# Kernel tuning notes

Hardware: AMD Instinct MI355X
Metric: run time of the kernel (lower is better)

## Reference

```python
import jax, jax.numpy as jnp
import numpy as np
import math

NX = 1024
N_HEAD = 16
HEAD_DIM = NX // N_HEAD
N_CTX = 2048
REL_VOCAB = 64
B = 2
S = 2048


def setup_inputs() -> dict:
    key = jax.random.key(0)
    ks = jax.random.split(key, 7)
    x = jax.random.normal(ks[0], (B, S, NX), dtype=jnp.float32)
    rel = jax.random.randint(ks[1], (B, S, S), 0, REL_VOCAB, dtype=jnp.int64)
    sc = 0.02
    Wqkv = jax.random.normal(ks[2], (NX, 3 * NX), dtype=jnp.float32) * sc
    bqkv = jnp.zeros((3 * NX,), dtype=jnp.float32)
    Wproj = jax.random.normal(ks[3], (NX, NX), dtype=jnp.float32) * sc
    bproj = jnp.zeros((NX,), dtype=jnp.float32)
    rel_emb = jax.random.normal(ks[4], (REL_VOCAB, N_HEAD), dtype=jnp.float32) * sc
    return {"x": x, "Wqkv": Wqkv, "bqkv": bqkv, "Wproj": Wproj,
            "bproj": bproj, "rel_emb": rel_emb, "rel": rel}


def reference(x, Wqkv, bqkv, Wproj, bproj, rel_emb, rel):
    Bsz, Sq, _ = x.shape
    qkv = x @ Wqkv + bqkv                      # [B,S,3*nx]
    q, k, v = jnp.split(qkv, 3, axis=-1)
    def split_heads(t):                        # [B,S,nx] -> [B,H,S,D]
        return t.reshape(Bsz, Sq, N_HEAD, HEAD_DIM).transpose(0, 2, 1, 3)
    q, k, v = split_heads(q), split_heads(k), split_heads(v)
    w = jnp.einsum('bhqd,bhkd->bhqk', q, k) / math.sqrt(HEAD_DIM)
    bmask = jnp.tril(jnp.ones((Sq, Sq), dtype=w.dtype))[None, None]  # [1,1,S,S]
    w = w * bmask - 1e10 * (1.0 - bmask)
    relw = rel_emb[rel].transpose(0, 3, 1, 2)  # [B,S,S,H] -> [B,H,S,S]
    w = w * (relw * bmask)                     # faithful: masked scores become 0
    p = jax.nn.softmax(w, axis=-1)
    a = jnp.einsum('bhqk,bhkd->bhqd', p, v)
    a = a.transpose(0, 2, 1, 3).reshape(Bsz, Sq, NX)  # merge heads
    return a @ Wproj + bproj
```

## Files before the change

### kernel.cpp

```cpp
#include <hip/hip_runtime.h>

typedef unsigned short u16;
typedef unsigned char u8;
typedef __attribute__((ext_vector_type(8))) short short8;
typedef __attribute__((ext_vector_type(4))) short short4v;
typedef __attribute__((ext_vector_type(4))) float f32x4;

#define GLD16(g, l) __builtin_amdgcn_global_load_lds( \
    (const __attribute__((address_space(1))) void*)(g), \
    (__attribute__((address_space(3))) void*)(l), 16, 0, 0)

__device__ __forceinline__ float bf2f(u16 u){
  union { unsigned int i; float f; } v; v.i = ((unsigned int)u) << 16; return v.f;
}
__device__ __forceinline__ u16 f2bf(float f){
  union { float f; unsigned int i; } v; v.f = f;
  unsigned int u = v.i;
  unsigned int r = (u + 0x7FFFu + ((u >> 16) & 1u)) >> 16;
  return (u16)r;
}

__device__ __forceinline__ f32x4 mfma16(short4v a, short4v b, f32x4 c){
#if __has_builtin(__builtin_amdgcn_mfma_f32_16x16x16bf16_1k)
  return __builtin_amdgcn_mfma_f32_16x16x16bf16_1k(a, b, c, 0, 0, 0);
#else
  asm volatile("s_nop 1\n\tv_mfma_f32_16x16x16_bf16 %0, %1, %2, %0" : "+v"(c) : "v"(a), "v"(b));
  return c;
#endif
}

__global__ __launch_bounds__(256) void prep_k(const float* __restrict__ x, u16* __restrict__ xb,
                                              const float* __restrict__ Wqkv, u16* __restrict__ wqkvT,
                                              const float* __restrict__ Wproj, u16* __restrict__ wprojT,
                                              const int* __restrict__ rel, u8* __restrict__ rel8){
  const int bid = blockIdx.x, t = threadIdx.x;
  if (bid < 4096){
    int i = bid * 256 + t;
    float4 v = ((const float4*)x)[i];
    unsigned long long pk = (unsigned long long)f2bf(v.x)
      | ((unsigned long long)f2bf(v.y) << 16)
      | ((unsigned long long)f2bf(v.z) << 32)
      | ((unsigned long long)f2bf(v.w) << 48);
    ((unsigned long long*)xb)[i] = pk;
  } else if (bid < 8192){
    const float* W; u16* Wt; int K, N, blk, nbx;
    if (bid < 7168){ W = Wqkv; Wt = wqkvT; K = 1024; N = 3072; blk = bid - 4096; nbx = 96; }
    else           { W = Wproj; Wt = wprojT; K = 1024; N = 1024; blk = bid - 7168; nbx = 32; }
    __shared__ float tl[32][33];
    int n0 = (blk % nbx) * 32, k0 = (blk / nbx) * 32;
    int tx = t & 31, ty = t >> 5;
    for (int i = ty; i < 32; i += 8)
      tl[i][tx] = W[(size_t)(k0 + i) * N + n0 + tx];
    __syncthreads();
    for (int i = ty; i < 32; i += 8)
      Wt[(size_t)(n0 + i) * K + k0 + tx] = f2bf(tl[tx][i]);
  } else {
    int i = (bid - 8192) * 256 + t;
    int4 v = ((const int4*)rel)[i];
    unsigned int pk = (unsigned int)(v.x & 255) | ((unsigned int)(v.y & 255) << 8)
      | ((unsigned int)(v.z & 255) << 16) | ((unsigned int)(v.w & 255) << 24);
    ((unsigned int*)rel8)[i] = pk;
  }
}

__global__ __launch_bounds__(256) void gemm_qkv_k(const u16* __restrict__ A, const u16* __restrict__ Bt,
                                                  const float* __restrict__ bias,
                                                  u16* __restrict__ oq, u16* __restrict__ okk, u16* __restrict__ vt){
  __shared__ u16 la[3][128 * 32];
  __shared__ u16 lb[3][128 * 32];
  const int K = 1024;
  const int t = threadIdx.x, w = t >> 6, lane = t & 63;
  const int l15 = lane & 15, l4 = lane >> 4;
  const int m0 = blockIdx.y * 128, n0 = blockIdx.x * 128;
  const int wr = w >> 1, wc = w & 1;
  f32x4 acc[4][4] = {};
  const u16* Abase = A + (size_t)m0 * K;
  const u16* Bbase = Bt + (size_t)n0 * K;

  const int srow0 = t >> 2, srow1 = 64 + (t >> 2);
  const int cg = t & 3;
  const int sc0 = cg ^ (srow0 & 3), sc1 = cg ^ (srow1 & 3);
  const int wbase0 = (w * 64) * 8, wbase1 = (256 + w * 64) * 8;

#define QSTAGE(kt, buf) do {                                                        \
    GLD16(Abase + (size_t)srow0 * K + (kt) * 32 + sc0 * 8, &la[buf][wbase0]);       \
    GLD16(Abase + (size_t)srow1 * K + (kt) * 32 + sc1 * 8, &la[buf][wbase1]);       \
    GLD16(Bbase + (size_t)srow0 * K + (kt) * 32 + sc0 * 8, &lb[buf][wbase0]);       \
    GLD16(Bbase + (size_t)srow1 * K + (kt) * 32 + sc1 * 8, &lb[buf][wbase1]);       \
  } while (0)

  QSTAGE(0, 0);
  QSTAGE(1, 1);
  for (int ki = 0; ki < 32; ++ki){
    __builtin_amdgcn_sched_barrier(0);
    if (ki < 31) asm volatile("s_waitcnt vmcnt(4)" ::: "memory");
    else         asm volatile("s_waitcnt vmcnt(0)" ::: "memory");
    __builtin_amdgcn_s_barrier();
    __builtin_amdgcn_sched_barrier(0);
    if (ki + 2 < 32) QSTAGE(ki + 2, (ki + 2) % 3);
    const int cb = ki % 3;
    short8 af[4], bfr[4];
#pragma unroll
    for (int mi = 0; mi < 4; ++mi){
      int row = wr * 64 + mi * 16 + l15;
      af[mi] = *(const short8*)&la[cb][row * 32 + ((l4 ^ (row & 3)) * 8)];
    }
#pragma unroll
    for (int ni = 0; ni < 4; ++ni){
      int row = wc * 64 + ni * 16 + l15;
      bfr[ni] = *(const short8*)&lb[cb][row * 32 + ((l4 ^ (row & 3)) * 8)];
    }
    __builtin_amdgcn_s_setprio(1);
#pragma unroll
    for (int mi = 0; mi < 4; ++mi)
#pragma unroll
      for (int ni = 0; ni < 4; ++ni)
        acc[mi][ni] = __builtin_amdgcn_mfma_f32_16x16x32_bf16(af[mi], bfr[ni], acc[mi][ni], 0, 0, 0);
    __builtin_amdgcn_s_setprio(0);
  }
#undef QSTAGE

#pragma unroll
  for (int mi = 0; mi < 4; ++mi){
    const int m_base = m0 + wr * 64 + mi * 16 + l4 * 4;
    const int bsel = m_base >> 11, s0q = m_base & 2047;
#pragma unroll
    for (int ni = 0; ni < 4; ++ni){
      int n = n0 + wc * 64 + ni * 16 + l15;
      float vb = bias[n];
      int tt = n >> 10, rr = n & 1023, head = rr >> 6, dd = rr & 63;
      if (tt == 2){
        int c = s0q >> 6, w6 = s0q & 63;
        int pj0 = (((w6 >> 2) & 3) << 4) | (((w6 >> 4) & 3) << 2);
        u16 o4[4];
#pragma unroll
        for (int r = 0; r < 4; ++r) o4[r] = f2bf(acc[mi][ni][r] + vb);
        *(uint2*)(vt + ((size_t)(bsel * 16 + head) * 64 + dd) * 2048 + c * 64 + pj0) = *(const uint2*)o4;
      } else {
        u16* dst = (tt == 0) ? oq : okk;
#pragma unroll
        for (int r = 0; r < 4; ++r)
          dst[(((size_t)(bsel * 16 + head)) * 2048 + s0q + r) * 64 + dd] = f2bf(acc[mi][ni][r] + vb);
      }
    }
  }
}

template<int BN>
__global__ __launch_bounds__(256) void gemm_bt_k(const u16* __restrict__ A, const u16* __restrict__ Bt,
                                                 const float* __restrict__ bias, float* __restrict__ of,
                                                 int M, int N, int K){
  __shared__ u16 la[128 * 64];
  __shared__ u16 lb[BN * 64];
  const int t = threadIdx.x, w = t >> 6, lane = t & 63;
  const int l15 = lane & 15, l4 = lane >> 4;
  const int m0 = blockIdx.y * 128, n0 = blockIdx.x * BN;
  const int wr = w >> 1, wc = w & 1;
  constexpr int NI = BN / 32;
  f32x4 acc[4][NI] = {};
  const u16* Abase = A + (size_t)m0 * K;
  const u16* Bbase = Bt + (size_t)n0 * K;
  for (int kt = 0; kt < K; kt += 64){
    __syncthreads();
#pragma unroll
    for (int i = 0; i < 4; ++i){
      int chunk = i * 256 + t;
      int row = chunk >> 3, cs = chunk & 7;
      int c = cs ^ (row & 7);
      GLD16(Abase + (size_t)row * K + kt + c * 8, &la[(i * 256 + w * 64) * 8]);
    }
#pragma unroll
    for (int i = 0; i < BN / 32; ++i){
      int chunk = i * 256 + t;
      int row = chunk >> 3, cs = chunk & 7;
      int c = cs ^ (row & 7);
      GLD16(Bbase + (size_t)row * K + kt + c * 8, &lb[(i * 256 + w * 64) * 8]);
    }
    asm volatile("s_waitcnt vmcnt(0)" ::: "memory");
    __syncthreads();
    short8 af[4][2], bfr[NI][2];
#pragma unroll
    for (int mi = 0; mi < 4; ++mi){
      int row = wr * 64 + mi * 16 + l15;
#pragma unroll
      for (int h = 0; h < 2; ++h)
        af[mi][h] = *(const short8*)&la[row * 64 + (((h * 4 + l4) ^ (row & 7)) * 8)];
    }
#pragma unroll
    for (int ni = 0; ni < NI; ++ni){
      int row = wc * (BN / 2) + ni * 16 + l15;
#pragma unroll
      for (int h = 0; h < 2; ++h)
        bfr[ni][h] = *(const short8*)&lb[row * 64 + (((h * 4 + l4) ^ (row & 7)) * 8)];
    }
#pragma unroll
    for (int mi = 0; mi < 4; ++mi)
#pragma unroll
      for (int ni = 0; ni < NI; ++ni){
        acc[mi][ni] = __builtin_amdgcn_mfma_f32_16x16x32_bf16(af[mi][0], bfr[ni][0], acc[mi][ni], 0, 0, 0);
        acc[mi][ni] = __builtin_amdgcn_mfma_f32_16x16x32_bf16(af[mi][1], bfr[ni][1], acc[mi][ni], 0, 0, 0);
      }
  }
#pragma unroll
  for (int mi = 0; mi < 4; ++mi){
#pragma unroll
    for (int ni = 0; ni < NI; ++ni){
#pragma unroll
      for (int r = 0; r < 4; ++r){
        int m = m0 + wr * 64 + mi * 16 + l4 * 4 + r;
        int n = n0 + wc * (BN / 2) + ni * 16 + l15;
        of[(size_t)m * N + n] = acc[mi][ni][r] + bias[n];
      }
    }
  }
}

__global__ __launch_bounds__(256) void vsuf2_k(const u16* __restrict__ vt, float* __restrict__ vsuf){
  __shared__ float part[32][64];
  const int bh = blockIdx.x;
  const int d = threadIdx.x & 63, qtr = threadIdx.x >> 6;
  const u16* row = vt + ((size_t)bh * 64 + d) * 2048;
  for (int c = qtr * 8; c < qtr * 8 + 8; ++c){
    float s = 0.f;
#pragma unroll
    for (int jv = 0; jv < 8; ++jv){
      short8 v = *(const short8*)(row + c * 64 + jv * 8);
#pragma unroll
      for (int e = 0; e < 8; ++e) s += bf2f((u16)v[e]);
    }
    part[c][d] = s;
  }
  __syncthreads();
  if (threadIdx.x < 64){
    float run = 0.f;
    vsuf[((size_t)bh * 33 + 32) * 64 + d] = 0.f;
    for (int c = 31; c >= 0; --c){
      run += part[c][d];
      vsuf[((size_t)bh * 33 + c) * 64 + d] = run;
    }
  }
}

template<int U8, int SPLIT>
__global__ __launch_bounds__(256, 4) void attn_k(const u16* __restrict__ qb, const u16* __restrict__ kb,
                                                 const u16* __restrict__ vt, const float* __restrict__ vsuf,
                                                 const void* __restrict__ relp, const float* __restrict__ rel_emb,
                                                 u16* __restrict__ ab, float* __restrict__ pacc,
                                                 float* __restrict__ prsum){
  __shared__ u16 Kt[2][64 * 64];
  __shared__ u16 Vt[2][64 * 64];
  __shared__ float remb[64];
  int p, hf, bh;
  if (SPLIT){
    const int lid = blockIdx.x;
    const int bhgrp = lid & 7, within = (lid >> 3) & 3, pf = lid >> 5;
    bh = bhgrp * 4 + within;
    p = pf >> 1; hf = pf & 1;
  } else {
    p = blockIdx.x; hf = 0; bh = blockIdx.y;
  }
  const int b = bh >> 4, h = bh & 15;
  const int TA = p, TB = 31 - p;
  const int q0A = TA * 64, q0B = TB * 64;
  const int tid = threadIdx.x, w = tid >> 6, lane = tid & 63;
  const int l15 = lane & 15, l4 = lane >> 4;
  if (tid < 64) remb[tid] = rel_emb[tid * 16 + h] * (0.125f * 1.44269504088896f);
  const u16* kbh = kb + ((size_t)bh * 2048) * 64;
  const u16* vbh = vt + ((size_t)bh * 64) * 2048;
  const u16* qA = qb + (((size_t)bh * 2048) + q0A + w * 16 + l15) * 64 + l4 * 8;
  const u16* qB = qb + (((size_t)bh * 2048) + q0B + w * 16 + l15) * 64 + l4 * 8;
  const short8 aqA0 = *(const short8*)qA, aqA1 = *(const short8*)(qA + 32);
  const short8 aqB0 = *(const short8*)qB, aqB1 = *(const short8*)(qB + 32);
  const u8*  r8A  = (const u8*)relp + ((size_t)b * 2048 + q0A + w * 16 + l15) * 2048;
  const u8*  r8B  = (const u8*)relp + ((size_t)b * 2048 + q0B + w * 16 + l15) * 2048;
  const int* r32A = (const int*)relp + ((size_t)b * 2048 + q0A + w * 16 + l15) * 2048;
  const int* r32B = (const int*)relp + ((size_t)b * 2048 + q0B + w * 16 + l15) * 2048;

  const int srow0 = (tid >> 3), srow1 = 32 + (tid >> 3);
  const int scs = tid & 7;
  const int sc0 = scs ^ (srow0 & 7), sc1 = scs ^ (srow1 & 7);
  const int sldsoff = (w * 64) * 8;

#define STAGE(ktile, buf) do {                                                       \
    GLD16(kbh + (size_t)((ktile) * 64 + srow0) * 64 + sc0 * 8, &Kt[buf][sldsoff]);   \
    GLD16(kbh + (size_t)((ktile) * 64 + srow1) * 64 + sc1 * 8, &Kt[buf][2048 + sldsoff]); \
    GLD16(vbh + (size_t)srow0 * 2048 + (ktile) * 64 + sc0 * 8, &Vt[buf][sldsoff]);   \
    GLD16(vbh + (size_t)srow1 * 2048 + (ktile) * 64 + sc1 * 8, &Vt[buf][2048 + sldsoff]); \
  } while (0)

  f32x4 acc[4] = {};
  float rsum = 0.f;
  unsigned int relc[4], reln[4];

  auto relload = [&](bool isA, int kt, unsigned int* dst){
    int off = kt * 64 + 4 * l4;
    if (U8){
      const u8* pp = isA ? r8A : r8B;
#pragma unroll
      for (int t = 0; t < 4; ++t) dst[t] = *(const unsigned int*)(pp + off + 16 * t);
    } else {
      const int* pp = isA ? r32A : r32B;
#pragma unroll
      for (int t = 0; t < 4; ++t){
        int4 v4 = *(const int4*)(pp + off + 16 * t);
        dst[t] = (unsigned int)(v4.x & 255) | ((unsigned int)(v4.y & 255) << 8)
               | ((unsigned int)(v4.z & 255) << 16) | ((unsigned int)(v4.w & 255) << 24);
      }
    }
  };

  auto writeout = [&](int Td, int q0){
    asm volatile("s_nop 7\n\ts_nop 7" :::);
    float s = rsum;
    s += __shfl_xor(s, 16);
    s += __shfl_xor(s, 32);
    float invZ = 1.f / (s + (float)(2048 - (Td + 1) * 64));
    int qg = q0 + w * 16 + l15;
    const float* sufp = vsuf + ((size_t)bh * 33 + Td + 1) * 64;
#pragma unroll
    for (int ni = 0; ni < 4; ++ni){
      float4 sv = *(const float4*)(sufp + ni * 16 + 4 * l4);
      unsigned int lo2 = (unsigned int)f2bf((acc[ni][0] + sv.x) * invZ)
                       | ((unsigned int)f2bf((acc[ni][1] + sv.y) * invZ) << 16);
      unsigned int hi2 = (unsigned int)f2bf((acc[ni][2] + sv.z) * invZ)
                       | ((unsigned int)f2bf((acc[ni][3] + sv.w) * invZ) << 16);
      uint2 o; o.x = lo2; o.y = hi2;
      *(uint2*)(ab + ((size_t)b * 2048 + qg) * 1024 + h * 64 + ni * 16 + 4 * l4) = o;
    }
  };

  const int lo = (SPLIT && hf) ? 17 : 0;
  const int hi = (SPLIT && !hf) ? 17 : 33;

  {
    bool isA0 = (lo <= TA);
    int kt0 = isA0 ? lo : lo - TA - 1;
    STAGE(kt0, 0);
    relload(isA0, kt0, relc);
  }

  for (int it = lo; it < hi; ++it){
    const bool isA = (it <= TA);
    const int kt = isA ? it : (it - TA - 1);
    const int cur = (it - lo) & 1;

    __builtin_amdgcn_sched_barrier(0);
    asm volatile("s_waitcnt vmcnt(4)" ::: "memory");
    __builtin_amdgcn_s_barrier();
    __builtin_amdgcn_sched_barrier(0);

    if (it + 1 < hi){
      const bool nA = (it + 1 <= TA);
      const int nkt = nA ? (it + 1) : (it - TA);
      STAGE(nkt, cur ^ 1);
      relload(nA, nkt, reln);
    }

    const short8 a0 = isA ? aqA0 : aqB0;
    const short8 a1 = isA ? aqA1 : aqB1;
    const bool diag = (kt == (isA ? TA : TB));

    short4v pk[4];
    __builtin_amdgcn_s_setprio(1);
#pragma unroll
    for (int t = 0; t < 4; ++t){
      const int krow = 16 * t + l15;
      const u16* kbase = &Kt[cur][krow * 64];
      short8 bk0 = *(const short8*)&kbase[((l4)     ^ (krow & 7)) * 8];
      short8 bk1 = *(const short8*)&kbase[((4 + l4) ^ (krow & 7)) * 8];
      f32x4 sf = {0.f, 0.f, 0.f, 0.f};
      sf = __builtin_amdgcn_mfma_f32_16x16x32_bf16(bk0, a0, sf, 0, 0, 0);
      sf = __builtin_amdgcn_mfma_f32_16x16x32_bf16(bk1, a1, sf, 0, 0, 0);
      unsigned int rw = relc[t];
      const int kk = 16 * t + 4 * l4;
      float prv[4];
#pragma unroll
      for (int r = 0; r < 4; ++r){
        float sc = sf[r] * remb[(rw >> (8 * r)) & 255];
        if (diag) sc = (kk + r <= w * 16 + l15) ? sc : 0.f;
        float pv = __builtin_amdgcn_exp2f(sc);
        rsum += pv;
        prv[r] = pv;
      }
      union { unsigned int u[2]; short4v s; } pu;
      asm("v_cvt_pk_bf16_f32 %0, %1, %2" : "=v"(pu.u[0]) : "v"(prv[0]), "v"(prv[1]));
      asm("v_cvt_pk_bf16_f32 %0, %1, %2" : "=v"(pu.u[1]) : "v"(prv[2]), "v"(prv[3]));
      pk[t] = pu.s;
    }
    asm volatile("s_nop 2" :::);
#pragma unroll
    for (int ni = 0; ni < 4; ++ni){
      const int drow = ni * 16 + l15;
      const u16* vbase = &Vt[cur][drow * 64];
      short8 vv0 = *(const short8*)&vbase[(((2 * l4)     ^ (drow & 7))) * 8];
      short8 vv1 = *(const short8*)&vbase[(((2 * l4 + 1) ^ (drow & 7))) * 8];
      short4v va0 = {vv0[0], vv0[1], vv0[2], vv0[3]};
      short4v va1 = {vv0[4], vv0[5], vv0[6], vv0[7]};
      short4v va2 = {vv1[0], vv1[1], vv1[2], vv1[3]};
      short4v va3 = {vv1[4], vv1[5], vv1[6], vv1[7]};
      acc[ni] = mfma16(va0, pk[0], acc[ni]);
      acc[ni] = mfma16(va1, pk[1], acc[ni]);
      acc[ni] = mfma16(va2, pk[2], acc[ni]);
      acc[ni] = mfma16(va3, pk[3], acc[ni]);
    }
    __builtin_amdgcn_s_setprio(0);

    if (it == TA){
      writeout(TA, q0A);
#pragma unroll
      for (int ni = 0; ni < 4; ++ni) acc[ni] = f32x4{0.f, 0.f, 0.f, 0.f};
      rsum = 0.f;
    }
    if (it + 1 < hi){
#pragma unroll
      for (int t = 0; t < 4; ++t) relc[t] = reln[t];
    }
  }
#undef STAGE

  if (SPLIT){
    asm volatile("s_nop 7\n\ts_nop 7" :::);
    float s = rsum;
    s += __shfl_xor(s, 16);
    s += __shfl_xor(s, 32);
    const size_t slot = (((size_t)bh * 16 + p) * 2 + hf);
    float* pslot = pacc + slot * 4096;
#pragma unroll
    for (int ni = 0; ni < 4; ++ni)
      *(f32x4*)(pslot + (w * 16 + l15) * 64 + ni * 16 + 4 * l4) = acc[ni];
    if (l4 == 0) prsum[slot * 64 + w * 16 + l15] = s;
  } else {
    writeout(TB, q0B);
  }
}

__global__ __launch_bounds__(256) void attn_fin_k(const float* __restrict__ pacc,
                                                  const float* __restrict__ prsum,
                                                  const float* __restrict__ vsuf,
                                                  u16* __restrict__ ab){
  const int p = blockIdx.x, bh = blockIdx.y;
  const int b = bh >> 4, h = bh & 15;
  const int TB = 31 - p, q0 = TB * 64;
  const int r = threadIdx.x >> 2, cg = threadIdx.x & 3;
  const size_t slot = ((size_t)bh * 16 + p) * 2;
  const size_t base = slot * 4096 + r * 64 + cg * 16;
  float rs = prsum[slot * 64 + r] + prsum[(slot + 1) * 64 + r];
  float invZ = 1.f / (rs + (float)(2048 - (TB + 1) * 64));
  const float* sufp = vsuf + ((size_t)bh * 33 + TB + 1) * 64 + cg * 16;
  u16 o[16];
#pragma unroll
  for (int j = 0; j < 4; ++j){
    f32x4 a0 = *(const f32x4*)(pacc + base + j * 4);
    f32x4 a1 = *(const f32x4*)(pacc + base + 4096 + j * 4);
    f32x4 sv = *(const f32x4*)(sufp + j * 4);
#pragma unroll
    for (int e = 0; e < 4; ++e) o[j * 4 + e] = f2bf((a0[e] + a1[e] + sv[e]) * invZ);
  }
  u16* dst = ab + ((size_t)b * 2048 + q0 + r) * 1024 + h * 64 + cg * 16;
  *(uint4*)dst = *(const uint4*)&o[0];
  *(uint4*)(dst + 8) = *(const uint4*)&o[8];
}

extern "C" void kernel_launch(void* const* d_in, const int* in_sizes, int n_in,
                              void* d_out, int out_size, void* d_ws, size_t ws_size,
                              hipStream_t stream){
  const float* x       = (const float*)d_in[0];
  const float* Wqkv    = (const float*)d_in[1];
  const float* bqkv    = (const float*)d_in[2];
  const float* Wproj   = (const float*)d_in[3];
  const float* bproj   = (const float*)d_in[4];
  const float* rel_emb = (const float*)d_in[5];
  const int*   rel     = (const int*)d_in[6];
  float* out = (float*)d_out;

  char* ws = (char*)d_ws;
  u16* xb     = (u16*)(ws);
  u16* wqkvT  = (u16*)(ws + (8ull  << 20));
  u16* wprojT = (u16*)(ws + (14ull << 20));
  u16* qb     = (u16*)(ws + (16ull << 20));
  u16* kb     = (u16*)(ws + (24ull << 20));
  u16* vtb    = (u16*)(ws + (40ull << 20));
  float* vsuf = (float*)(ws + (48ull << 20));
  float* pacc = (float*)(ws + (49ull << 20));
  float* prsum= (float*)(ws + (65ull << 20) + (512ull << 10));
  u8*   rel8  = (u8*)(ws + (66ull << 20));
  const bool useSplit = ws_size >= (67ull << 20);
  const bool useU8    = ws_size >= (75ull << 20);

  prep_k<<<useU8 ? 16384 : 8192, 256, 0, stream>>>(x, xb, Wqkv, wqkvT, Wproj, wprojT, rel, rel8);
  gemm_qkv_k<<<dim3(24, 32), 256, 0, stream>>>(xb, wqkvT, bqkv, qb, kb, vtb);
  vsuf2_k<<<32, 256, 0, stream>>>(vtb, vsuf);
  if (useU8)
    attn_k<1, 1><<<dim3(1024), 256, 0, stream>>>(qb, kb, vtb, vsuf, rel8, rel_emb, xb, pacc, prsum);
  else if (useSplit)
    attn_k<0, 1><<<dim3(1024), 256, 0, stream>>>(qb, kb, vtb, vsuf, rel, rel_emb, xb, pacc, prsum);
  else
    attn_k<0, 0><<<dim3(16, 32), 256, 0, stream>>>(qb, kb, vtb, vsuf, rel, rel_emb, xb, pacc, prsum);
  if (useSplit || useU8)
    attn_fin_k<<<dim3(16, 32), 256, 0, stream>>>(pacc, prsum, vsuf, xb);
  gemm_bt_k<64><<<dim3(16, 32), 256, 0, stream>>>(xb, wprojT, bproj, out, 4096, 1024, 1024);
}
```

Baseline: 138.6 us.

## Use 128-row query blocks with 8 waves sharing each K/V tile

The attention kernel now runs 512-thread blocks that each own 128 query rows (8 waves) instead of 64 rows. Every staged 64-key K/V tile is reused by twice as many waves, which halves global K/V traffic per query, and each thread now stages one 16-byte chunk per matrix instead of two. Diagonal masking is generalised with a tile-relative offset, and the split partial buffers and the finishing kernel are resized to 128-row slots. In exchange the grid has half as many blocks, and the prefetch wait is now a full vmcnt(0), which may expose load latency that was previously hidden.

```diff
diff --git a/kernel.cpp b/kernel.cpp
--- a/kernel.cpp
+++ b/kernel.cpp
@@ -242,7 +242,7 @@
 }
 
 template<int U8, int SPLIT>
-__global__ __launch_bounds__(256, 4) void attn_k(const u16* __restrict__ qb, const u16* __restrict__ kb,
+__global__ __launch_bounds__(512, 2) void attn_k(const u16* __restrict__ qb, const u16* __restrict__ kb,
                                                  const u16* __restrict__ vt, const float* __restrict__ vsuf,
                                                  const void* __restrict__ relp, const float* __restrict__ rel_emb,
                                                  u16* __restrict__ ab, float* __restrict__ pacc,
@@ -260,8 +260,8 @@
     p = blockIdx.x; hf = 0; bh = blockIdx.y;
   }
   const int b = bh >> 4, h = bh & 15;
-  const int TA = p, TB = 31 - p;
-  const int q0A = TA * 64, q0B = TB * 64;
+  const int TAe = 2 * p + 1, TBe = 31 - 2 * p;
+  const int q0A = p * 128, q0B = (15 - p) * 128;
   const int tid = threadIdx.x, w = tid >> 6, lane = tid & 63;
   const int l15 = lane & 15, l4 = lane >> 4;
   if (tid < 64) remb[tid] = rel_emb[tid * 16 + h] * (0.125f * 1.44269504088896f);
@@ -276,16 +276,13 @@
   const int* r32A = (const int*)relp + ((size_t)b * 2048 + q0A + w * 16 + l15) * 2048;
   const int* r32B = (const int*)relp + ((size_t)b * 2048 + q0B + w * 16 + l15) * 2048;
 
-  const int srow0 = (tid >> 3), srow1 = 32 + (tid >> 3);
-  const int scs = tid & 7;
-  const int sc0 = scs ^ (srow0 & 7), sc1 = scs ^ (srow1 & 7);
+  const int srow = tid >> 3;
+  const int sc = (tid & 7) ^ (srow & 7);
   const int sldsoff = (w * 64) * 8;
 
-#define STAGE(ktile, buf) do {                                                       \
-    GLD16(kbh + (size_t)((ktile) * 64 + srow0) * 64 + sc0 * 8, &Kt[buf][sldsoff]);   \
-    GLD16(kbh + (size_t)((ktile) * 64 + srow1) * 64 + sc1 * 8, &Kt[buf][2048 + sldsoff]); \
-    GLD16(vbh + (size_t)srow0 * 2048 + (ktile) * 64 + sc0 * 8, &Vt[buf][sldsoff]);   \
-    GLD16(vbh + (size_t)srow1 * 2048 + (ktile) * 64 + sc1 * 8, &Vt[buf][2048 + sldsoff]); \
+#define STAGE(ktile, buf) do {                                                      \
+    GLD16(kbh + (size_t)((ktile) * 64 + srow) * 64 + sc * 8, &Kt[buf][sldsoff]);    \
+    GLD16(vbh + (size_t)srow * 2048 + (ktile) * 64 + sc * 8, &Vt[buf][sldsoff]);    \
   } while (0)
 
   f32x4 acc[4] = {};
@@ -309,14 +306,14 @@
     }
   };
 
-  auto writeout = [&](int Td, int q0){
+  auto writeout = [&](int Te, int q0){
     asm volatile("s_nop 7\n\ts_nop 7" :::);
     float s = rsum;
     s += __shfl_xor(s, 16);
     s += __shfl_xor(s, 32);
-    float invZ = 1.f / (s + (float)(2048 - (Td + 1) * 64));
+    float invZ = 1.f / (s + (float)(2048 - (Te + 1) * 64));
     int qg = q0 + w * 16 + l15;
-    const float* sufp = vsuf + ((size_t)bh * 33 + Td + 1) * 64;
+    const float* sufp = vsuf + ((size_t)bh * 33 + Te + 1) * 64;
 #pragma unroll
     for (int ni = 0; ni < 4; ++ni){
       float4 sv = *(const float4*)(sufp + ni * 16 + 4 * l4);
@@ -329,36 +326,50 @@
     }
   };
 
+  auto emitP = [&](){
+    asm volatile("s_nop 7\n\ts_nop 7" :::);
+    float s = rsum;
+    s += __shfl_xor(s, 16);
+    s += __shfl_xor(s, 32);
+    const size_t slot = (((size_t)bh * 8 + p) * 2 + hf);
+    float* pslot = pacc + slot * 8192 + (size_t)(w * 16 + l15) * 64;
+#pragma unroll
+    for (int ni = 0; ni < 4; ++ni)
+      *(f32x4*)(pslot + ni * 16 + 4 * l4) = acc[ni];
+    if (l4 == 0) prsum[slot * 128 + w * 16 + l15] = s;
+  };
+
   const int lo = (SPLIT && hf) ? 17 : 0;
-  const int hi = (SPLIT && !hf) ? 17 : 33;
+  const int hi = (SPLIT && !hf) ? 17 : 34;
 
   {
-    bool isA0 = (lo <= TA);
-    int kt0 = isA0 ? lo : lo - TA - 1;
+    bool isA0 = (lo <= TAe);
+    int kt0 = isA0 ? lo : lo - TAe - 1;
     STAGE(kt0, 0);
     relload(isA0, kt0, relc);
   }
 
   for (int it = lo; it < hi; ++it){
-    const bool isA = (it <= TA);
-    const int kt = isA ? it : (it - TA - 1);
+    const bool isA = (it <= TAe);
+    const int kt = isA ? it : (it - TAe - 1);
     const int cur = (it - lo) & 1;
 
     __builtin_amdgcn_sched_barrier(0);
-    asm volatile("s_waitcnt vmcnt(4)" ::: "memory");
+    asm volatile("s_waitcnt vmcnt(0)" ::: "memory");
     __builtin_amdgcn_s_barrier();
     __builtin_amdgcn_sched_barrier(0);
 
     if (it + 1 < hi){
-      const bool nA = (it + 1 <= TA);
-      const int nkt = nA ? (it + 1) : (it - TA);
+      const bool nA = (it + 1 <= TAe);
+      const int nkt = nA ? (it + 1) : (it - TAe);
       STAGE(nkt, cur ^ 1);
       relload(nA, nkt, reln);
     }
 
     const short8 a0 = isA ? aqA0 : aqB0;
     const short8 a1 = isA ? aqA1 : aqB1;
-    const bool diag = (kt == (isA ? TA : TB));
+    const int kbase_rel = kt * 64 - (isA ? q0A : q0B);
+    const bool diag = (kbase_rel >= 0);
 
     short4v pk[4];
     __builtin_amdgcn_s_setprio(1);
@@ -376,9 +387,9 @@
       float prv[4];
 #pragma unroll
       for (int r = 0; r < 4; ++r){
-        float sc = sf[r] * remb[(rw >> (8 * r)) & 255];
-        if (diag) sc = (kk + r <= w * 16 + l15) ? sc : 0.f;
-        float pv = __builtin_amdgcn_exp2f(sc);
+        float sc2 = sf[r] * remb[(rw >> (8 * r)) & 255];
+        if (diag) sc2 = (kbase_rel + kk + r <= w * 16 + l15) ? sc2 : 0.f;
+        float pv = __builtin_amdgcn_exp2f(sc2);
         rsum += pv;
         prv[r] = pv;
       }
@@ -405,8 +416,8 @@
     }
     __builtin_amdgcn_s_setprio(0);
 
-    if (it == TA){
-      writeout(TA, q0A);
+    if (it == TAe){
+      writeout(TAe, q0A);
 #pragma unroll
       for (int ni = 0; ni < 4; ++ni) acc[ni] = f32x4{0.f, 0.f, 0.f, 0.f};
       rsum = 0.f;
@@ -418,20 +429,8 @@
   }
 #undef STAGE
 
-  if (SPLIT){
-    asm volatile("s_nop 7\n\ts_nop 7" :::);
-    float s = rsum;
-    s += __shfl_xor(s, 16);
-    s += __shfl_xor(s, 32);
-    const size_t slot = (((size_t)bh * 16 + p) * 2 + hf);
-    float* pslot = pacc + slot * 4096;
-#pragma unroll
-    for (int ni = 0; ni < 4; ++ni)
-      *(f32x4*)(pslot + (w * 16 + l15) * 64 + ni * 16 + 4 * l4) = acc[ni];
-    if (l4 == 0) prsum[slot * 64 + w * 16 + l15] = s;
-  } else {
-    writeout(TB, q0B);
-  }
+  if (SPLIT) emitP();
+  else       writeout(TBe, q0B);
 }
 
 __global__ __launch_bounds__(256) void attn_fin_k(const float* __restrict__ pacc,
@@ -440,25 +439,30 @@
                                                   u16* __restrict__ ab){
   const int p = blockIdx.x, bh = blockIdx.y;
   const int b = bh >> 4, h = bh & 15;
-  const int TB = 31 - p, q0 = TB * 64;
-  const int r = threadIdx.x >> 2, cg = threadIdx.x & 3;
-  const size_t slot = ((size_t)bh * 16 + p) * 2;
-  const size_t base = slot * 4096 + r * 64 + cg * 16;
-  float rs = prsum[slot * 64 + r] + prsum[(slot + 1) * 64 + r];
-  float invZ = 1.f / (rs + (float)(2048 - (TB + 1) * 64));
-  const float* sufp = vsuf + ((size_t)bh * 33 + TB + 1) * 64 + cg * 16;
-  u16 o[16];
-#pragma unroll
-  for (int j = 0; j < 4; ++j){
-    f32x4 a0 = *(const f32x4*)(pacc + base + j * 4);
-    f32x4 a1 = *(const f32x4*)(pacc + base + 4096 + j * 4);
+  const int TBe = 31 - 2 * p;
+  const int q0 = (15 - p) * 128;
+  const int r = threadIdx.x >> 1;
+  const int dh = (threadIdx.x & 1) * 32;
+  const size_t slot = ((size_t)bh * 8 + p) * 2;
+  const float* p0 = pacc + slot * 8192 + (size_t)r * 64 + dh;
+  const float* p1 = p0 + 8192;
+  float rs = prsum[slot * 128 + r] + prsum[(slot + 1) * 128 + r];
+  float invZ = 1.f / (rs + (float)(2048 - (TBe + 1) * 64));
+  const float* sufp = vsuf + ((size_t)bh * 33 + TBe + 1) * 64 + dh;
+  u16 o[32];
+#pragma unroll
+  for (int j = 0; j < 8; ++j){
+    f32x4 a0 = *(const f32x4*)(p0 + j * 4);
+    f32x4 a1 = *(const f32x4*)(p1 + j * 4);
     f32x4 sv = *(const f32x4*)(sufp + j * 4);
 #pragma unroll
     for (int e = 0; e < 4; ++e) o[j * 4 + e] = f2bf((a0[e] + a1[e] + sv[e]) * invZ);
   }
-  u16* dst = ab + ((size_t)b * 2048 + q0 + r) * 1024 + h * 64 + cg * 16;
+  u16* dst = ab + ((size_t)b * 2048 + q0 + r) * 1024 + h * 64 + dh;
   *(uint4*)dst = *(const uint4*)&o[0];
   *(uint4*)(dst + 8) = *(const uint4*)&o[8];
+  *(uint4*)(dst + 16) = *(const uint4*)&o[16];
+  *(uint4*)(dst + 24) = *(const uint4*)&o[24];
 }
 
 extern "C" void kernel_launch(void* const* d_in, const int* in_sizes, int n_in,
@@ -490,13 +494,13 @@
   prep_k<<<useU8 ? 16384 : 8192, 256, 0, stream>>>(x, xb, Wqkv, wqkvT, Wproj, wprojT, rel, rel8);
   gemm_qkv_k<<<dim3(24, 32), 256, 0, stream>>>(xb, wqkvT, bqkv, qb, kb, vtb);
   vsuf2_k<<<32, 256, 0, stream>>>(vtb, vsuf);
-  if (useU8)
-    attn_k<1, 1><<<dim3(1024), 256, 0, stream>>>(qb, kb, vtb, vsuf, rel8, rel_emb, xb, pacc, prsum);
-  else if (useSplit)
-    attn_k<0, 1><<<dim3(1024), 256, 0, stream>>>(qb, kb, vtb, vsuf, rel, rel_emb, xb, pacc, prsum);
-  else
-    attn_k<0, 0><<<dim3(16, 32), 256, 0, stream>>>(qb, kb, vtb, vsuf, rel, rel_emb, xb, pacc, prsum);
-  if (useSplit || useU8)
-    attn_fin_k<<<dim3(16, 32), 256, 0, stream>>>(pacc, prsum, vsuf, xb);
+  if (useU8 && useSplit){
+    attn_k<1, 1><<<dim3(512), 512, 0, stream>>>(qb, kb, vtb, vsuf, rel8, rel_emb, xb, pacc, prsum);
+    attn_fin_k<<<dim3(8, 32), 256, 0, stream>>>(pacc, prsum, vsuf, xb);
+  } else if (useU8){
+    attn_k<1, 0><<<dim3(8, 32), 512, 0, stream>>>(qb, kb, vtb, vsuf, rel8, rel_emb, xb, pacc, prsum);
+  } else {
+    attn_k<0, 0><<<dim3(8, 32), 512, 0, stream>>>(qb, kb, vtb, vsuf, rel, rel_emb, xb, pacc, prsum);
+  }
   gemm_bt_k<64><<<dim3(16, 32), 256, 0, stream>>>(xb, wprojT, bproj, out, 4096, 1024, 1024);
 }
```

After: 140.9 us. Within noise of the previous version (+1.6%).
